# Kernel optimization log

Hardware: AMD Instinct MI355X
Metric: run time of the kernel (lower is better)

## Reference

```python
import jax, jax.numpy as jnp
import numpy as np
from jax import lax

DIM = 64
HEADS = 4
B, H, W = 4, 256, 256


def _conv(x, w, b, pad, groups=1):
    y = lax.conv_general_dilated(x, w, (1, 1), [(pad, pad), (pad, pad)],
                                 dimension_numbers=('NCHW', 'OIHW', 'NCHW'),
                                 feature_group_count=groups)
    return y + b[None, :, None, None]


def _ckbd_mask(h, w, anchor):
    ii = jnp.arange(h)[:, None]
    jj = jnp.arange(w)[None, :]
    par = (ii + jj) % 2
    return (par == 1) if anchor else (par == 0)


def ckbd_anchor(y):
    return y * _ckbd_mask(y.shape[2], y.shape[3], True)


def ckbd_nonanchor(y):
    return y * _ckbd_mask(y.shape[2], y.shape[3], False)


def anchor_squeeze(y):
    b, c, h, w = y.shape
    even = y[:, :, 0::2, 1::2]  # anchor cells on even rows
    odd = y[:, :, 1::2, 0::2]   # anchor cells on odd rows
    return jnp.stack([even, odd], axis=3).reshape(b, c, h, w // 2)


def nonanchor_squeeze(y):
    b, c, h, w = y.shape
    even = y[:, :, 0::2, 0::2]
    odd = y[:, :, 1::2, 1::2]
    return jnp.stack([even, odd], axis=3).reshape(b, c, h, w // 2)


def anchor_unsqueeze(y):
    b, c, h, wh = y.shape
    out = jnp.zeros((b, c, h, wh * 2), y.dtype)
    out = out.at[:, :, 0::2, 1::2].set(y[:, :, 0::2, :])
    out = out.at[:, :, 1::2, 0::2].set(y[:, :, 1::2, :])
    return out


def nonanchor_unsqueeze(y):
    b, c, h, wh = y.shape
    out = jnp.zeros((b, c, h, wh * 2), y.dtype)
    out = out.at[:, :, 0::2, 0::2].set(y[:, :, 0::2, :])
    out = out.at[:, :, 1::2, 1::2].set(y[:, :, 1::2, :])
    return out


def setup_inputs() -> dict:
    key = jax.random.key(0)
    ks = jax.random.split(key, 16)
    s = 0.05
    C = DIM
    nrm = lambda k, shp: jax.random.normal(k, shp, jnp.float32) * s
    z = lambda n: jnp.zeros((n,), jnp.float32)
    return {
        'x1': jax.random.normal(ks[0], (B, C, H, W), jnp.float32),
        'x2': jax.random.normal(ks[1], (B, C, H, W), jnp.float32),
        'q1_w': nrm(ks[2], (C, C, 1, 1)), 'q1_b': z(C),
        'q2_w': nrm(ks[3], (C, 1, 3, 3)), 'q2_b': z(C),
        'k1_w': nrm(ks[4], (C, C, 1, 1)), 'k1_b': z(C),
        'k2_w': nrm(ks[5], (C, 1, 3, 3)), 'k2_b': z(C),
        'v1_w': nrm(ks[6], (C, C, 1, 1)), 'v1_b': z(C),
        'v2_w': nrm(ks[7], (C, 1, 3, 3)), 'v2_b': z(C),
        'r_w': nrm(ks[8], (2 * C, C, 5, 5)), 'r_b': z(2 * C),
        'm1_w': nrm(ks[9], (4 * C, 2 * C, 1, 1)), 'm1_b': z(4 * C),
        'm2_w': nrm(ks[10], (4 * C, 1, 3, 3)), 'm2_b': z(4 * C),
        'm3_w': nrm(ks[11], (2 * C, 4 * C, 1, 1)), 'm3_b': z(2 * C),
    }


def reference(x1, x2, q1_w, q1_b, q2_w, q2_b, k1_w, k1_b, k2_w, k2_b,
              v1_w, v1_b, v2_w, v2_b, r_w, r_b,
              m1_w, m1_b, m2_w, m2_b, m3_w, m3_b):
    C = DIM
    b, _, h, w = x1.shape
    d = C // HEADS
    x1_ac = ckbd_anchor(x1)
    x1_na = ckbd_nonanchor(x1)
    # QKV: 1x1 conv then depthwise 3x3
    q = _conv(_conv(x1_na, q1_w, q1_b, 0), q2_w, q2_b, 1, groups=C)
    k = _conv(_conv(x1_ac, k1_w, k1_b, 0), k2_w, k2_b, 1, groups=C)
    v = _conv(_conv(x2, v1_w, v1_b, 0), v2_w, v2_b, 1, groups=C)
    q = nonanchor_squeeze(q)  # (b, C, h, w//2)
    k = anchor_squeeze(k)
    v = anchor_squeeze(v)
    # per-head softmaxes: key over spatial, query over head channels
    kh = k.reshape(b, HEADS, d, h * (w // 2))
    qh = q.reshape(b, HEADS, d, h, w // 2)
    kh = jax.nn.softmax(kh, axis=-1).reshape(b, HEADS, d, h, w // 2)
    qh = jax.nn.softmax(qh, axis=2)
    vh = v.reshape(b, HEADS, d, h, w // 2)
    # scatter back to full grid (zeros off-pattern), flatten spatial
    kf = anchor_unsqueeze(kh.reshape(b, C, h, w // 2)).reshape(b, HEADS, d, h * w)
    vf = anchor_unsqueeze(vh.reshape(b, C, h, w // 2)).reshape(b, HEADS, d, h * w)
    qf = nonanchor_unsqueeze(qh.reshape(b, C, h, w // 2)).reshape(b, HEADS, d, h * w)
    # linear attention: context = K @ V^T (d x d), out = context^T @ Q
    ctx = jnp.einsum('bhdn,bhen->bhde', kf, vf)
    att = jnp.einsum('bhde,bhdn->bhen', ctx, qf).reshape(b, C, h, w)
    attention = _conv(att, r_w, r_b, 2)
    m = jax.nn.gelu(_conv(attention, m1_w, m1_b, 0), approximate=False)
    m = jax.nn.gelu(_conv(m, m2_w, m2_b, 1, groups=4 * C), approximate=False)
    m = _conv(m, m3_w, m3_b, 0)
    return attention + m
```

## Files before the change

kernel.cpp:

```cpp
#include <hip/hip_runtime.h>
#include <hip/hip_bf16.h>
#include <cstdint>

#define NHW 65536
#define NSQ 32768

static constexpr size_t OFF_AQ  = 0;
static constexpr size_t OFF_AK  = 8388608;
static constexpr size_t OFF_AV  = 16777216;
static constexpr size_t OFF_EK  = 33554432;
static constexpr size_t OFF_VD  = 41943040;
static constexpr size_t OFF_ATT = 50331648;
static constexpr size_t OFF_CTX = 58720256;
static constexpr size_t OFF_Z   = 58724352;
static constexpr size_t OFF_RWT = 58724608;
static constexpr size_t MB2_US  = 67108864;
static constexpr size_t A16_US  = 67108864;
static constexpr size_t W6_US   = 117654016;
static constexpr size_t W8_US   = 0;

typedef __attribute__((ext_vector_type(8))) short short8;
typedef __attribute__((ext_vector_type(4))) float floatx4;

__device__ __constant__ int TKH[25] = {0,0,0,1,1,2,2,2,3,3,4,4,4,  0,0,1,1,1,2,2,3,3,3,4,4};
__device__ __constant__ int TKW[25] = {0,2,4,1,3,0,2,4,1,3,0,2,4,  1,3,0,2,4,1,3,0,2,4,1,3};

__device__ __forceinline__ float geluf(float x) {
  return 0.5f * x * (1.0f + erff(x * 0.70710678118654752440f));
}
__device__ __forceinline__ unsigned short f2bf(float f) {
  union { float f; uint32_t u; } v; v.f = f;
  uint32_t x = v.u;
  uint32_t r = x + 0x7fffu + ((x >> 16) & 1u);
  return (unsigned short)(r >> 16);
}
__device__ __forceinline__ float bf2f(unsigned short u) {
  union { uint32_t i; float f; } v; v.i = ((uint32_t)u) << 16; return v.f;
}

__global__ void __launch_bounds__(256) k0_wprep(const float* __restrict__ rw,
                                                unsigned short* __restrict__ wAu) {
  int idx = blockIdx.x * 256 + threadIdx.x;
  int cj = idx & 7, o = (idx >> 3) & 127, chunk = (idx >> 10) & 7, tap = idx >> 13;
  int c = chunk * 8 + cj;
  int t = TKH[tap] * 5 + TKW[tap];
  wAu[idx] = f2bf(rw[(o * 64 + c) * 25 + t]);
}

__global__ void __launch_bounds__(256) k0b_w6(const float* __restrict__ m1w,
                                              unsigned short* __restrict__ w6) {
  int idx = blockIdx.x * 256 + threadIdx.x;
  int cj = idx & 7, o = (idx >> 3) & 255, chunk = idx >> 11;
  w6[idx] = f2bf(m1w[o * 128 + chunk * 8 + cj]);
}

__global__ void __launch_bounds__(256) k0c_w8(const float* __restrict__ m3w,
                                              unsigned short* __restrict__ w8) {
  int idx = blockIdx.x * 256 + threadIdx.x;
  int cj = idx & 7, o = (idx >> 3) & 127, chunk = idx >> 10;
  w8[idx] = f2bf(m3w[o * 256 + chunk * 8 + cj]);
}

__global__ void __launch_bounds__(256) k1_qkv(
    const float* __restrict__ x1, const float* __restrict__ x2,
    const float* __restrict__ q1w, const float* __restrict__ q1b,
    const float* __restrict__ k1w, const float* __restrict__ k1b,
    const float* __restrict__ v1w, const float* __restrict__ v1b,
    float* ws) {
  __shared__ float wq[4096], wk[4096], wv[4096];
  int tid = threadIdx.x;
  for (int idx = tid; idx < 4096; idx += 256) {
    int o = idx >> 6, c = idx & 63;
    wq[c * 64 + o] = q1w[o * 64 + c];
    wk[c * 64 + o] = k1w[o * 64 + c];
    wv[c * 64 + o] = v1w[o * 64 + c];
  }
  __syncthreads();
  int b = blockIdx.x >> 8, i = blockIdx.x & 255;
  int w = tid >> 6, l = tid & 63;
  int j = (((w >> 1) * 64 + l) << 1) | (w & 1);
  int par = (i + j) & 1;
  const float* wsel = par ? wk : wq;
  const float* bsel = par ? k1b : q1b;
  float acc[64];
#pragma unroll
  for (int o = 0; o < 64; o++) acc[o] = bsel[o];
  const float* xp = x1 + ((size_t)b * 64) * NHW + i * 256 + j;
  for (int c = 0; c < 64; c++) {
    float v = xp[(size_t)c * NHW];
    const float* wr = wsel + c * 64;
#pragma unroll
    for (int o = 0; o < 64; o++) acc[o] += wr[o] * v;
  }
  {
    float* dst = ws + (par ? OFF_AK : OFF_AQ) + ((size_t)b * 64) * NSQ + i * 128 + (j >> 1);
#pragma unroll
    for (int o = 0; o < 64; o++) dst[(size_t)o * NSQ] = acc[o];
  }
#pragma unroll
  for (int o = 0; o < 64; o++) acc[o] = v1b[o];
  const float* xp2 = x2 + ((size_t)b * 64) * NHW + i * 256 + j;
  for (int c = 0; c < 64; c++) {
    float v = xp2[(size_t)c * NHW];
    const float* wr = wv + c * 64;
#pragma unroll
    for (int o = 0; o < 64; o++) acc[o] += wr[o] * v;
  }
  float* dv = ws + OFF_AV + ((size_t)b * 64) * NHW + i * 256 + j;
#pragma unroll
  for (int o = 0; o < 64; o++) dv[(size_t)o * NHW] = acc[o];
}

__global__ void __launch_bounds__(256) k2_dw(
    float* ws,
    const float* __restrict__ kw2, const float* __restrict__ kb2, const float* __restrict__ kb1,
    const float* __restrict__ vw2, const float* __restrict__ vb2) {
  int ig = blockIdx.x, c = blockIdx.y, b = blockIdx.z;
  int i0 = ig * 16;
  int tid = threadIdx.x;

  __shared__ float akL[18][130];
  __shared__ float avL[18][260];
  __shared__ float red[256];

  const float* AKg = ws + OFF_AK + ((size_t)(b * 64 + c)) * NSQ;
  const float* AVg = ws + OFF_AV + ((size_t)(b * 64 + c)) * NHW;

  for (int idx = tid; idx < 18 * 128; idx += 256) {
    int r = idx >> 7, col = idx & 127;
    int gi = i0 - 1 + r;
    akL[r][1 + col] = (gi >= 0 && gi < 256) ? AKg[gi * 128 + col] : 0.f;
  }
  for (int idx = tid; idx < 18 * 256; idx += 256) {
    int r = idx >> 8, col = idx & 255;
    int gi = i0 - 1 + r;
    avL[r][1 + col] = (gi >= 0 && gi < 256) ? AVg[gi * 256 + col] : 0.f;
  }
  if (tid < 18) {
    akL[tid][0] = 0.f; akL[tid][129] = 0.f;
    avL[tid][0] = 0.f; avL[tid][257] = 0.f;
  }
  __syncthreads();

  int tr = tid >> 4, tj = tid & 15;
  int i = i0 + tr;
  int jp0 = tj * 8;
  int li = tr + 1;
  int s = 1 - (i & 1);

  const float* w9 = kw2 + c * 9;
  float kw0 = w9[0], kw1 = w9[1], kw2c = w9[2], kw3 = w9[3], kw4 = w9[4],
        kw5 = w9[5], kw6 = w9[6], kw7 = w9[7], kw8 = w9[8];
  float kb2c = kb2[c], kb1c = kb1[c];
  const float* vwp = vw2 + c * 9;
  float vw0 = vwp[0], vw1 = vwp[1], vw2v = vwp[2], vw3 = vwp[3], vw4 = vwp[4],
        vw5 = vwp[5], vw6 = vwp[6], vw7 = vwp[7], vw8 = vwp[8];
  float vbc = vb2[c];

  float ek[8], vd[8];
  float zsum = 0.f;
#pragma unroll
  for (int u = 0; u < 8; u++) {
    int jp = jp0 + u;
    int j = 2 * jp + s;
    float bs = 0.f;
    if (i > 0)   bs += kw1;
    if (i < 255) bs += kw7;
    if (j > 0)   bs += kw3;
    if (j < 255) bs += kw5;
    float acc = kb2c + kb1c * bs
      + kw4 * akL[li][1 + jp]
      + kw0 * akL[li - 1][jp + s] + kw2c * akL[li - 1][1 + jp + s]
      + kw6 * akL[li + 1][jp + s] + kw8 * akL[li + 1][1 + jp + s];
    float e = expf(acc);
    ek[u] = e; zsum += e;
    vd[u] = vbc
      + vw0 * avL[li - 1][j] + vw1 * avL[li - 1][1 + j] + vw2v * avL[li - 1][2 + j]
      + vw3 * avL[li    ][j] + vw4 * avL[li    ][1 + j] + vw5  * avL[li    ][2 + j]
      + vw6 * avL[li + 1][j] + vw7 * avL[li + 1][1 + j] + vw8  * avL[li + 1][2 + j];
  }

  float* ekp = ws + OFF_EK + ((size_t)(b * 64 + c)) * NSQ + i * 128 + jp0;
  float* vdp = ws + OFF_VD + ((size_t)(b * 64 + c)) * NSQ + i * 128 + jp0;
  float4 e0 = {ek[0], ek[1], ek[2], ek[3]}, e1 = {ek[4], ek[5], ek[6], ek[7]};
  float4 v0 = {vd[0], vd[1], vd[2], vd[3]}, v1 = {vd[4], vd[5], vd[6], vd[7]};
  *(float4*)(ekp) = e0; *(float4*)(ekp + 4) = e1;
  *(float4*)(vdp) = v0; *(float4*)(vdp + 4) = v1;

  red[tid] = zsum;
  __syncthreads();
#pragma unroll
  for (int off = 128; off > 0; off >>= 1) {
    if (tid < off) red[tid] += red[tid + off];
    __syncthreads();
  }
  if (tid == 0) atomicAdd(ws + OFF_Z + (b * 64 + c), red[0]);
}

__global__ void __launch_bounds__(256) k3_ctx(float* ws) {
  int bid = blockIdx.x;
  int b = bid >> 5, h = (bid >> 3) & 3, ch = bid & 7;
  int n0 = ch * 4096;
  int tid = threadIdx.x;
  int d = tid >> 4, e = tid & 15;
  __shared__ float ekt[16][260];
  __shared__ float vdt[16][260];
  const float* ekb = ws + OFF_EK + ((size_t)(b * 64 + h * 16)) * NSQ + n0;
  const float* vdb = ws + OFF_VD + ((size_t)(b * 64 + h * 16)) * NSQ + n0;
  float acc = 0.f;
  for (int sub = 0; sub < 16; sub++) {
    __syncthreads();
#pragma unroll
    for (int r = 0; r < 16; r++) {
      ekt[r][tid] = ekb[(size_t)r * NSQ + sub * 256 + tid];
      vdt[r][tid] = vdb[(size_t)r * NSQ + sub * 256 + tid];
    }
    __syncthreads();
#pragma unroll 8
    for (int x = 0; x < 256; x++) acc += ekt[d][x] * vdt[e][x];
  }
  atomicAdd(ws + OFF_CTX + ((b * 4 + h) * 16 + d) * 16 + e, acc);
}

__global__ void __launch_bounds__(256) k4_att(
    float* ws,
    const float* __restrict__ qw2, const float* __restrict__ qb2, const float* __restrict__ qb1) {
  int b = blockIdx.x >> 7, ip = blockIdx.x & 127;
  int tid = threadIdx.x;
  int i = ip * 2 + (tid >> 7);
  int jp = tid & 127;
  __shared__ float ctxn[1024];
  for (int idx = tid; idx < 1024; idx += 256)
    ctxn[idx] = ws[OFF_CTX + b * 1024 + idx] / ws[OFF_Z + b * 64 + (idx >> 4)];
  __syncthreads();
  int s = i & 1;
  int j = 2 * jp + s;
  int cl = jp - 1 + s, cr = jp + s;
  unsigned short* attB = (unsigned short*)(ws + OFF_ATT);
  unsigned short* dstp = attB + (((size_t)(b * 256 + i)) * 128 + jp) * 64;
  for (int h = 0; h < 4; h++) {
    float qv[16];
#pragma unroll
    for (int dc = 0; dc < 16; dc++) {
      int c = h * 16 + dc;
      const float* AQ = ws + OFF_AQ + ((size_t)(b * 64 + c)) * NSQ;
      const float* w9 = qw2 + c * 9;
      float acc = qb2[c] + w9[4] * AQ[i * 128 + jp];
      if (i > 0) {
        const float* r = AQ + (i - 1) * 128;
        if (cl >= 0)   acc += w9[0] * r[cl];
        if (cr <= 127) acc += w9[2] * r[cr];
      }
      if (i < 255) {
        const float* r = AQ + (i + 1) * 128;
        if (cl >= 0)   acc += w9[6] * r[cl];
        if (cr <= 127) acc += w9[8] * r[cr];
      }
      float bs = 0.f;
      if (i > 0)   bs += w9[1];
      if (i < 255) bs += w9[7];
      if (j > 0)   bs += w9[3];
      if (j < 255) bs += w9[5];
      qv[dc] = acc + qb1[c] * bs;
    }
    float mx = qv[0];
#pragma unroll
    for (int dc = 1; dc < 16; dc++) mx = fmaxf(mx, qv[dc]);
    float sum = 0.f;
#pragma unroll
    for (int dc = 0; dc < 16; dc++) { qv[dc] = expf(qv[dc] - mx); sum += qv[dc]; }
    float inv = 1.0f / sum;
#pragma unroll
    for (int e = 0; e < 16; e++) {
      float a = 0.f;
#pragma unroll
      for (int dc = 0; dc < 16; dc++) a += ctxn[h * 256 + dc * 16 + e] * qv[dc];
      dstp[h * 16 + e] = f2bf(a * inv);
    }
  }
}

__global__ void __launch_bounds__(256) k5_mfma(
    const unsigned short* __restrict__ attB, const unsigned short* __restrict__ wAu,
    const float* __restrict__ rb, float* __restrict__ out,
    unsigned short* __restrict__ a16) {
  int p = blockIdx.y, b = blockIdx.z;
  int i0 = (blockIdx.x >> 2) * 4;
  int jp0 = (blockIdx.x & 3) * 32;
  int tid = threadIdx.x;
  int wv = tid >> 6, lane = tid & 63;
  int mh = wv & 1, nh = wv >> 1;
  int l15 = lane & 15, quad = lane >> 4;

  __shared__ __align__(16) unsigned short attL[24576];
  __shared__ __align__(16) unsigned short wL[8192];

  const unsigned short* attBase = attB + ((size_t)b * 256) * 128 * 64;
  for (int k = 0; k < 12; k++) {
    int u = k * 256 + tid;
    int chunk = u & 7;
    int pos = (u >> 3) & 15;
    int cbr = u >> 7;
    int cb = cbr % 3, lr = cbr / 3;
    int r = i0 - 2 + lr;
    int jp = jp0 - 2 + cb * 16 + pos;
    short8 v = {0, 0, 0, 0, 0, 0, 0, 0};
    if (r >= 0 && r < 256 && jp >= 0 && jp < 128)
      v = *(const short8*)(attBase + (((size_t)r * 128) + jp) * 64 + chunk * 8);
    int slot = chunk ^ (pos & 7);
    *(short8*)(attL + (((size_t)cbr * 16 + pos) * 8 + slot) * 8) = v;
  }

  floatx4 acc[16];
#pragma unroll
  for (int x = 0; x < 16; x++) acc[x] = floatx4{0.f, 0.f, 0.f, 0.f};

  int riv[4], ci2[4];
#pragma unroll
  for (int nt = 0; nt < 4; nt++) {
    int ntg = nh * 4 + nt;
    riv[nt] = ntg >> 1;
    ci2[nt] = (ntg & 1) * 16 + l15 + 2;
  }

  int t0 = p ? 13 : 0;
  int ntaps = p ? 12 : 13;
  for (int tt = 0; tt < ntaps; tt++) {
    int tap = t0 + tt;
    int kh = TKH[tap], kw = TKW[tap];
    __syncthreads();
    {
      const short8* src = (const short8*)(wAu + (size_t)tap * 8192);
      short8* dst = (short8*)wL;
#pragma unroll
      for (int k = 0; k < 4; k++) dst[k * 256 + tid] = src[k * 256 + tid];
    }
    __syncthreads();
#pragma unroll
    for (int chalf = 0; chalf < 2; chalf++) {
      short8 a[4], bf[4];
#pragma unroll
      for (int mt = 0; mt < 4; mt++)
        a[mt] = *(const short8*)(wL + (((chalf * 4 + quad) * 128) + mh * 64 + mt * 16 + l15) * 8);
#pragma unroll
      for (int nt = 0; nt < 4; nt++) {
        int lr = riv[nt] + kh;
        int off = ((kw - 2) + ((p + riv[nt]) & 1) - ((riv[nt] + kh) & 1)) >> 1;
        int lc = ci2[nt] + off;
        int cb = lc >> 4, pos = lc & 15;
        int slot = (chalf * 4 + quad) ^ (pos & 7);
        bf[nt] = *(const short8*)(attL + ((((lr * 3 + cb) * 16 + pos) * 8) + slot) * 8);
      }
#pragma unroll
      for (int mt = 0; mt < 4; mt++)
#pragma unroll
        for (int nt = 0; nt < 4; nt++)
          acc[mt * 4 + nt] =
              __builtin_amdgcn_mfma_f32_16x16x32_bf16(a[mt], bf[nt], acc[mt * 4 + nt], 0, 0, 0);
    }
  }

#pragma unroll
  for (int mt = 0; mt < 4; mt++) {
#pragma unroll
    for (int nt = 0; nt < 4; nt++) {
      int ntg = nh * 4 + nt;
      int i = i0 + (ntg >> 1);
      int jp = jp0 + (ntg & 1) * 16 + l15;
      int j = 2 * jp + ((p + i) & 1);
      floatx4 v = acc[mt * 4 + nt];
      int o0 = mh * 64 + mt * 16 + quad * 4;
      ushort4 u4;
      float r0 = v[0] + rb[o0 + 0];
      float r1 = v[1] + rb[o0 + 1];
      float r2 = v[2] + rb[o0 + 2];
      float r3 = v[3] + rb[o0 + 3];
      out[(((size_t)(b * 128 + o0 + 0)) * 256 + i) * 256 + j] = r0;
      out[(((size_t)(b * 128 + o0 + 1)) * 256 + i) * 256 + j] = r1;
      out[(((size_t)(b * 128 + o0 + 2)) * 256 + i) * 256 + j] = r2;
      out[(((size_t)(b * 128 + o0 + 3)) * 256 + i) * 256 + j] = r3;
      u4.x = f2bf(r0); u4.y = f2bf(r1); u4.z = f2bf(r2); u4.w = f2bf(r3);
      *(ushort4*)(a16 + ((size_t)b * 65536 + (size_t)i * 256 + j) * 128 + o0) = u4;
    }
  }
}

__global__ void __launch_bounds__(256) k6_m1(
    const unsigned short* __restrict__ a16, const unsigned short* __restrict__ w6,
    const float* __restrict__ m1b, unsigned short* __restrict__ mb) {
  int px0 = blockIdx.x * 128;
  int og = blockIdx.y, b = blockIdx.z;
  int tid = threadIdx.x;
  int wv = tid >> 6, lane = tid & 63;
  int mh = wv & 1, nh = wv >> 1;
  int l15 = lane & 15, quad = lane >> 4;
  __shared__ __align__(16) unsigned short attL[16384];

  const unsigned short* src = a16 + ((size_t)b * 65536 + px0) * 128;
#pragma unroll
  for (int k = 0; k < 8; k++) {
    int u = k * 256 + tid;
    int n = u >> 4, chunk = u & 15;
    short8 v = *(const short8*)(src + (size_t)n * 128 + chunk * 8);
    int slot = chunk ^ (n & 7);
    *(short8*)(attL + ((size_t)n * 16 + slot) * 8) = v;
  }
  __syncthreads();

  floatx4 acc[16];
#pragma unroll
  for (int x = 0; x < 16; x++) acc[x] = floatx4{0.f, 0.f, 0.f, 0.f};

#pragma unroll
  for (int step = 0; step < 4; step++) {
    int chunk = step * 4 + quad;
    short8 aw[4], bp[4];
#pragma unroll
    for (int mt = 0; mt < 4; mt++) {
      int o = og * 128 + mh * 64 + mt * 16 + l15;
      aw[mt] = *(const short8*)(w6 + ((size_t)chunk * 256 + o) * 8);
    }
#pragma unroll
    for (int nt = 0; nt < 4; nt++) {
      int row = nh * 64 + nt * 16 + l15;
      int slot = chunk ^ (row & 7);
      bp[nt] = *(const short8*)(attL + (row * 16 + slot) * 8);
    }
#pragma unroll
    for (int mt = 0; mt < 4; mt++)
#pragma unroll
      for (int nt = 0; nt < 4; nt++)
        acc[mt * 4 + nt] =
            __builtin_amdgcn_mfma_f32_16x16x32_bf16(aw[mt], bp[nt], acc[mt * 4 + nt], 0, 0, 0);
  }

#pragma unroll
  for (int mt = 0; mt < 4; mt++) {
    int o0 = og * 128 + mh * 64 + mt * 16 + quad * 4;
    float4 bo = *(const float4*)(m1b + o0);
#pragma unroll
    for (int nt = 0; nt < 4; nt++) {
      int px = px0 + nh * 64 + nt * 16 + l15;
      floatx4 v = acc[mt * 4 + nt];
      ushort4 u;
      u.x = f2bf(geluf(v[0] + bo.x));
      u.y = f2bf(geluf(v[1] + bo.y));
      u.z = f2bf(geluf(v[2] + bo.z));
      u.w = f2bf(geluf(v[3] + bo.w));
      *(ushort4*)(mb + ((size_t)b * 65536 + px) * 256 + o0) = u;
    }
  }
}

__global__ void __launch_bounds__(256) k7_m2(
    const unsigned short* __restrict__ mb, const float* __restrict__ m2w,
    const float* __restrict__ m2b, unsigned short* __restrict__ mb2) {
  int b = blockIdx.y;
  int i0 = (blockIdx.x >> 2) * 4;
  int jq = blockIdx.x & 3;
  int t = threadIdx.x;
  int l = t & 63, ri = t >> 6;
  int co = l * 4;
  int i = i0 + ri;
  int j0 = jq * 64;
  const unsigned short* ibase = mb + ((size_t)b * 65536) * 256 + co;
  unsigned short* obase = mb2 + ((size_t)b * 65536) * 256 + co;

  float w[9][4], bias[4];
#pragma unroll
  for (int cc = 0; cc < 4; cc++) {
    bias[cc] = m2b[co + cc];
#pragma unroll
    for (int tap = 0; tap < 9; tap++) w[tap][cc] = m2w[(co + cc) * 9 + tap];
  }

  float wA[3][4], wB[3][4], wC[3][4];

#define K7_LOAD(dst, ir, jc)                                                        \
  do {                                                                              \
    if ((unsigned)(ir) < 256u && (unsigned)(jc) < 256u) {                           \
      ushort4 u_ = *(const ushort4*)(ibase + ((size_t)((ir) * 256 + (jc))) * 256);  \
      dst[0] = bf2f(u_.x); dst[1] = bf2f(u_.y);                                     \
      dst[2] = bf2f(u_.z); dst[3] = bf2f(u_.w);                                     \
    } else {                                                                        \
      dst[0] = 0.f; dst[1] = 0.f; dst[2] = 0.f; dst[3] = 0.f;                       \
    }                                                                               \
  } while (0)

#pragma unroll
  for (int r = 0; r < 3; r++) {
    K7_LOAD(wA[r], i - 1 + r, j0 - 1);
    K7_LOAD(wB[r], i - 1 + r, j0);
  }

  for (int j = j0; j < j0 + 64; j++) {
#pragma unroll
    for (int r = 0; r < 3; r++) K7_LOAD(wC[r], i - 1 + r, j + 1);
    float acc[4];
#pragma unroll
    for (int cc = 0; cc < 4; cc++) {
      acc[cc] = bias[cc]
        + w[0][cc] * wA[0][cc] + w[1][cc] * wB[0][cc] + w[2][cc] * wC[0][cc]
        + w[3][cc] * wA[1][cc] + w[4][cc] * wB[1][cc] + w[5][cc] * wC[1][cc]
        + w[6][cc] * wA[2][cc] + w[7][cc] * wB[2][cc] + w[8][cc] * wC[2][cc];
    }
    ushort4 u;
    u.x = f2bf(geluf(acc[0]));
    u.y = f2bf(geluf(acc[1]));
    u.z = f2bf(geluf(acc[2]));
    u.w = f2bf(geluf(acc[3]));
    *(ushort4*)(obase + ((size_t)(i * 256 + j)) * 256) = u;
#pragma unroll
    for (int r = 0; r < 3; r++) {
#pragma unroll
      for (int cc = 0; cc < 4; cc++) { wA[r][cc] = wB[r][cc]; wB[r][cc] = wC[r][cc]; }
    }
  }
#undef K7_LOAD
}

__global__ void __launch_bounds__(256) k8_m3(
    const unsigned short* __restrict__ mb2, const unsigned short* __restrict__ w8,
    const float* __restrict__ m3b, float* __restrict__ out) {
  int px0 = blockIdx.x * 128;
  int b = blockIdx.z;
  int tid = threadIdx.x;
  int wv = tid >> 6, lane = tid & 63;
  int mh = wv & 1, nh = wv >> 1;
  int l15 = lane & 15, quad = lane >> 4;
  __shared__ __align__(16) unsigned short attL[16384];

  floatx4 acc[16];
#pragma unroll
  for (int x = 0; x < 16; x++) acc[x] = floatx4{0.f, 0.f, 0.f, 0.f};

  for (int kk = 0; kk < 2; kk++) {
    if (kk) __syncthreads();
    const unsigned short* src = mb2 + ((size_t)b * 65536 + px0) * 256 + kk * 128;
#pragma unroll
    for (int k = 0; k < 8; k++) {
      int u = k * 256 + tid;
      int n = u >> 4, ch = u & 15;
      short8 v = *(const short8*)(src + (size_t)n * 256 + ch * 8);
      int slot = ch ^ (n & 7);
      *(short8*)(attL + ((size_t)n * 16 + slot) * 8) = v;
    }
    __syncthreads();

#pragma unroll
    for (int step = 0; step < 4; step++) {
      int ch = step * 4 + quad;
      int chg = kk * 16 + ch;
      short8 aw[4], bp[4];
#pragma unroll
      for (int mt = 0; mt < 4; mt++) {
        int o = mh * 64 + mt * 16 + l15;
        aw[mt] = *(const short8*)(w8 + ((size_t)chg * 128 + o) * 8);
      }
#pragma unroll
      for (int nt = 0; nt < 4; nt++) {
        int row = nh * 64 + nt * 16 + l15;
        int slot = ch ^ (row & 7);
        bp[nt] = *(const short8*)(attL + (row * 16 + slot) * 8);
      }
#pragma unroll
      for (int mt = 0; mt < 4; mt++)
#pragma unroll
        for (int nt = 0; nt < 4; nt++)
          acc[mt * 4 + nt] =
              __builtin_amdgcn_mfma_f32_16x16x32_bf16(aw[mt], bp[nt], acc[mt * 4 + nt], 0, 0, 0);
    }
  }

#pragma unroll
  for (int mt = 0; mt < 4; mt++) {
    int o0 = mh * 64 + mt * 16 + quad * 4;
    float4 bo = *(const float4*)(m3b + o0);
#pragma unroll
    for (int nt = 0; nt < 4; nt++) {
      int px = px0 + nh * 64 + nt * 16 + l15;
      floatx4 v = acc[mt * 4 + nt];
      size_t a0 = ((size_t)(b * 128 + o0 + 0)) * NHW + px;
      size_t a1 = ((size_t)(b * 128 + o0 + 1)) * NHW + px;
      size_t a2 = ((size_t)(b * 128 + o0 + 2)) * NHW + px;
      size_t a3 = ((size_t)(b * 128 + o0 + 3)) * NHW + px;
      out[a0] += v[0] + bo.x;
      out[a1] += v[1] + bo.y;
      out[a2] += v[2] + bo.z;
      out[a3] += v[3] + bo.w;
    }
  }
}

extern "C" void kernel_launch(void* const* d_in, const int* in_sizes, int n_in,
                              void* d_out, int out_size, void* d_ws, size_t ws_size,
                              hipStream_t stream) {
  const float* x1  = (const float*)d_in[0];
  const float* x2  = (const float*)d_in[1];
  const float* q1w = (const float*)d_in[2];  const float* q1b = (const float*)d_in[3];
  const float* q2w = (const float*)d_in[4];  const float* q2b = (const float*)d_in[5];
  const float* k1w = (const float*)d_in[6];  const float* k1b = (const float*)d_in[7];
  const float* k2w = (const float*)d_in[8];  const float* k2b = (const float*)d_in[9];
  const float* v1w = (const float*)d_in[10]; const float* v1b = (const float*)d_in[11];
  const float* v2w = (const float*)d_in[12]; const float* v2b = (const float*)d_in[13];
  const float* rw  = (const float*)d_in[14]; const float* rb  = (const float*)d_in[15];
  const float* m1w = (const float*)d_in[16]; const float* m1b = (const float*)d_in[17];
  const float* m2w = (const float*)d_in[18]; const float* m2b = (const float*)d_in[19];
  const float* m3w = (const float*)d_in[20]; const float* m3b = (const float*)d_in[21];
  float* ws = (float*)d_ws;
  float* out = (float*)d_out;
  unsigned short* mb  = (unsigned short*)d_ws;
  unsigned short* mb2 = (unsigned short*)d_ws + MB2_US;
  unsigned short* a16 = (unsigned short*)d_ws + A16_US;
  unsigned short* w6  = (unsigned short*)d_ws + W6_US;
  unsigned short* w8  = (unsigned short*)d_ws + W8_US;
  unsigned short* attB = (unsigned short*)(ws + OFF_ATT);
  unsigned short* wAu  = (unsigned short*)(ws + OFF_RWT);

  (void)hipMemsetAsync((char*)d_ws + OFF_CTX * sizeof(float), 0, (4096 + 256) * sizeof(float), stream);
  k0_wprep<<<800, 256, 0, stream>>>(rw, wAu);
  k0b_w6<<<128, 256, 0, stream>>>(m1w, w6);
  k1_qkv<<<1024, 256, 0, stream>>>(x1, x2, q1w, q1b, k1w, k1b, v1w, v1b, ws);
  k2_dw<<<dim3(16, 64, 4), 256, 0, stream>>>(ws, k2w, k2b, k1b, v2w, v2b);
  k3_ctx<<<128, 256, 0, stream>>>(ws);
  k4_att<<<512, 256, 0, stream>>>(ws, q2w, q2b, q1b);
  k5_mfma<<<dim3(256, 2, 4), 256, 0, stream>>>(attB, wAu, rb, out, a16);
  k6_m1<<<dim3(512, 2, 4), 256, 0, stream>>>(a16, w6, m1b, mb);
  k7_m2<<<dim3(256, 4), 256, 0, stream>>>(mb, m2w, m2b, mb2);
  k0c_w8<<<128, 256, 0, stream>>>(m3w, w8);
  k8_m3<<<dim3(512, 1, 4), 256, 0, stream>>>(mb2, w8, m3b, out);
}
```

Baseline: 1.004 ms.

## Rewrite QKV 1x1 projections as bf16 MFMA GEMMs with swizzled LDS tiles

Replaces the scalar fp32 per-thread 64-channel dot products in the QKV projection kernel with bf16 MFMA 16x16x32 matrix ops. Input rows are converted to bf16 and staged in a XOR-swizzled LDS tile, and weights are pre-converted to bf16 by a new prep kernel. Q and K are computed only on their checkerboard-selected columns. This targets the FMA-bound, register-heavy original loop, but lowers projection precision to bf16 and adds a small prep launch.

New measurement: 931.3 us. 7.3% less time.

```diff
diff --git a/kernel.cpp b/kernel.cpp
--- a/kernel.cpp
+++ b/kernel.cpp
@@ -17,6 +17,7 @@
 static constexpr size_t MB2_US  = 67108864;
 static constexpr size_t A16_US  = 67108864;
 static constexpr size_t W6_US   = 117654016;
+static constexpr size_t WQKV_US = 117686784;
 static constexpr size_t W8_US   = 0;
 
 typedef __attribute__((ext_vector_type(8))) short short8;
@@ -61,54 +62,157 @@
   w8[idx] = f2bf(m3w[o * 256 + chunk * 8 + cj]);
 }
 
+__global__ void __launch_bounds__(256) k0d_wqkv(
+    const float* __restrict__ q1w, const float* __restrict__ k1w,
+    const float* __restrict__ v1w, unsigned short* __restrict__ wqkv) {
+  int idx = blockIdx.x * 256 + threadIdx.x;
+  int cj = idx & 7, o = (idx >> 3) & 63, chunk = (idx >> 9) & 7, mat = idx >> 12;
+  const float* src = mat == 0 ? q1w : (mat == 1 ? k1w : v1w);
+  wqkv[idx] = f2bf(src[o * 64 + chunk * 8 + cj]);
+}
+
 __global__ void __launch_bounds__(256) k1_qkv(
     const float* __restrict__ x1, const float* __restrict__ x2,
-    const float* __restrict__ q1w, const float* __restrict__ q1b,
-    const float* __restrict__ k1w, const float* __restrict__ k1b,
-    const float* __restrict__ v1w, const float* __restrict__ v1b,
-    float* ws) {
-  __shared__ float wq[4096], wk[4096], wv[4096];
+    const unsigned short* __restrict__ wqkv,
+    const float* __restrict__ q1b, const float* __restrict__ k1b,
+    const float* __restrict__ v1b, float* ws) {
+  int b = blockIdx.x >> 8, i = blockIdx.x & 255;
   int tid = threadIdx.x;
-  for (int idx = tid; idx < 4096; idx += 256) {
-    int o = idx >> 6, c = idx & 63;
-    wq[c * 64 + o] = q1w[o * 64 + c];
-    wk[c * 64 + o] = k1w[o * 64 + c];
-    wv[c * 64 + o] = v1w[o * 64 + c];
+  int wv = tid >> 6, lane = tid & 63;
+  int mh = wv & 1, nh = wv >> 1;
+  int l15 = lane & 15, quad = lane >> 4;
+  __shared__ __align__(16) unsigned short xL[16384];
+
+  {
+    const float* xr = x1 + ((size_t)b * 64) * NHW + i * 256;
+#pragma unroll
+    for (int u = 0; u < 8; u++) {
+      int idx = u * 256 + tid;
+      int j = idx & 255, chunk = idx >> 8;
+      short8 v;
+#pragma unroll
+      for (int cj = 0; cj < 8; cj++)
+        v[cj] = (short)f2bf(xr[(size_t)(chunk * 8 + cj) * NHW + j]);
+      int slot = chunk ^ ((j >> 1) & 7);
+      *(short8*)(xL + (size_t)(j * 8 + slot) * 8) = v;
+    }
   }
   __syncthreads();
-  int b = blockIdx.x >> 8, i = blockIdx.x & 255;
-  int w = tid >> 6, l = tid & 63;
-  int j = (((w >> 1) * 64 + l) << 1) | (w & 1);
-  int par = (i + j) & 1;
-  const float* wsel = par ? wk : wq;
-  const float* bsel = par ? k1b : q1b;
-  float acc[64];
-#pragma unroll
-  for (int o = 0; o < 64; o++) acc[o] = bsel[o];
-  const float* xp = x1 + ((size_t)b * 64) * NHW + i * 256 + j;
-  for (int c = 0; c < 64; c++) {
-    float v = xp[(size_t)c * NHW];
-    const float* wr = wsel + c * 64;
-#pragma unroll
-    for (int o = 0; o < 64; o++) acc[o] += wr[o] * v;
-  }
+
+  int s_na = i & 1, s_a = 1 - s_na;
+
+  floatx4 accq[8], acck[8];
+#pragma unroll
+  for (int x = 0; x < 8; x++) {
+    accq[x] = floatx4{0.f, 0.f, 0.f, 0.f};
+    acck[x] = floatx4{0.f, 0.f, 0.f, 0.f};
+  }
+
+#pragma unroll
+  for (int chalf = 0; chalf < 2; chalf++) {
+    int chunk = chalf * 4 + quad;
+    short8 awq[2], awk[2], bq[4], bk[4];
+#pragma unroll
+    for (int mt = 0; mt < 2; mt++) {
+      int o = mh * 32 + mt * 16 + l15;
+      awq[mt] = *(const short8*)(wqkv + ((size_t)(0 * 8 + chunk) * 64 + o) * 8);
+      awk[mt] = *(const short8*)(wqkv + ((size_t)(1 * 8 + chunk) * 64 + o) * 8);
+    }
+#pragma unroll
+    for (int nt = 0; nt < 4; nt++) {
+      int jp = nh * 64 + nt * 16 + l15;
+      int slot = chunk ^ (jp & 7);
+      int jq = 2 * jp + s_na, jk = 2 * jp + s_a;
+      bq[nt] = *(const short8*)(xL + (size_t)(jq * 8 + slot) * 8);
+      bk[nt] = *(const short8*)(xL + (size_t)(jk * 8 + slot) * 8);
+    }
+#pragma unroll
+    for (int mt = 0; mt < 2; mt++)
+#pragma unroll
+      for (int nt = 0; nt < 4; nt++) {
+        accq[mt * 4 + nt] =
+            __builtin_amdgcn_mfma_f32_16x16x32_bf16(awq[mt], bq[nt], accq[mt * 4 + nt], 0, 0, 0);
+        acck[mt * 4 + nt] =
+            __builtin_amdgcn_mfma_f32_16x16x32_bf16(awk[mt], bk[nt], acck[mt * 4 + nt], 0, 0, 0);
+      }
+  }
+
+#pragma unroll
+  for (int mt = 0; mt < 2; mt++) {
+    int o0 = mh * 32 + mt * 16 + quad * 4;
+    float4 bq4 = *(const float4*)(q1b + o0);
+    float4 bk4 = *(const float4*)(k1b + o0);
+#pragma unroll
+    for (int nt = 0; nt < 4; nt++) {
+      int jp = nh * 64 + nt * 16 + l15;
+      floatx4 vq = accq[mt * 4 + nt];
+      floatx4 vk = acck[mt * 4 + nt];
+      float* dq = ws + OFF_AQ + ((size_t)(b * 64 + o0)) * NSQ + i * 128 + jp;
+      float* dk = ws + OFF_AK + ((size_t)(b * 64 + o0)) * NSQ + i * 128 + jp;
+      dq[0 * NSQ] = vq[0] + bq4.x; dq[1 * NSQ] = vq[1] + bq4.y;
+      dq[2 * NSQ] = vq[2] + bq4.z; dq[3 * NSQ] = vq[3] + bq4.w;
+      dk[0 * NSQ] = vk[0] + bk4.x; dk[1 * NSQ] = vk[1] + bk4.y;
+      dk[2 * NSQ] = vk[2] + bk4.z; dk[3 * NSQ] = vk[3] + bk4.w;
+    }
+  }
+
+  __syncthreads();
   {
-    float* dst = ws + (par ? OFF_AK : OFF_AQ) + ((size_t)b * 64) * NSQ + i * 128 + (j >> 1);
-#pragma unroll
-    for (int o = 0; o < 64; o++) dst[(size_t)o * NSQ] = acc[o];
-  }
-#pragma unroll
-  for (int o = 0; o < 64; o++) acc[o] = v1b[o];
-  const float* xp2 = x2 + ((size_t)b * 64) * NHW + i * 256 + j;
-  for (int c = 0; c < 64; c++) {
-    float v = xp2[(size_t)c * NHW];
-    const float* wr = wv + c * 64;
-#pragma unroll
-    for (int o = 0; o < 64; o++) acc[o] += wr[o] * v;
-  }
-  float* dv = ws + OFF_AV + ((size_t)b * 64) * NHW + i * 256 + j;
-#pragma unroll
-  for (int o = 0; o < 64; o++) dv[(size_t)o * NHW] = acc[o];
+    const float* xr = x2 + ((size_t)b * 64) * NHW + i * 256;
+#pragma unroll
+    for (int u = 0; u < 8; u++) {
+      int idx = u * 256 + tid;
+      int j = idx & 255, chunk = idx >> 8;
+      short8 v;
+#pragma unroll
+      for (int cj = 0; cj < 8; cj++)
+        v[cj] = (short)f2bf(xr[(size_t)(chunk * 8 + cj) * NHW + j]);
+      int slot = chunk ^ ((j >> 1) & 7);
+      *(short8*)(xL + (size_t)(j * 8 + slot) * 8) = v;
+    }
+  }
+  __syncthreads();
+
+  floatx4 accv[16];
+#pragma unroll
+  for (int x = 0; x < 16; x++) accv[x] = floatx4{0.f, 0.f, 0.f, 0.f};
+
+#pragma unroll
+  for (int chalf = 0; chalf < 2; chalf++) {
+    int chunk = chalf * 4 + quad;
+    short8 awv[2], bv[8];
+#pragma unroll
+    for (int mt = 0; mt < 2; mt++) {
+      int o = mh * 32 + mt * 16 + l15;
+      awv[mt] = *(const short8*)(wqkv + ((size_t)(2 * 8 + chunk) * 64 + o) * 8);
+    }
+#pragma unroll
+    for (int nt = 0; nt < 8; nt++) {
+      int j = nh * 128 + nt * 16 + l15;
+      int slot = chunk ^ ((j >> 1) & 7);
+      bv[nt] = *(const short8*)(xL + (size_t)(j * 8 + slot) * 8);
+    }
+#pragma unroll
+    for (int mt = 0; mt < 2; mt++)
+#pragma unroll
+      for (int nt = 0; nt < 8; nt++)
+        accv[mt * 8 + nt] =
+            __builtin_amdgcn_mfma_f32_16x16x32_bf16(awv[mt], bv[nt], accv[mt * 8 + nt], 0, 0, 0);
+  }
+
+#pragma unroll
+  for (int mt = 0; mt < 2; mt++) {
+    int o0 = mh * 32 + mt * 16 + quad * 4;
+    float4 bv4 = *(const float4*)(v1b + o0);
+#pragma unroll
+    for (int nt = 0; nt < 8; nt++) {
+      int j = nh * 128 + nt * 16 + l15;
+      floatx4 vv = accv[mt * 8 + nt];
+      float* dv = ws + OFF_AV + ((size_t)(b * 64 + o0)) * NHW + i * 256 + j;
+      dv[0 * NHW] = vv[0] + bv4.x; dv[1 * NHW] = vv[1] + bv4.y;
+      dv[2 * NHW] = vv[2] + bv4.z; dv[3 * NHW] = vv[3] + bv4.w;
+    }
+  }
 }
 
 __global__ void __launch_bounds__(256) k2_dw(
@@ -613,6 +717,7 @@
   unsigned short* mb2 = (unsigned short*)d_ws + MB2_US;
   unsigned short* a16 = (unsigned short*)d_ws + A16_US;
   unsigned short* w6  = (unsigned short*)d_ws + W6_US;
+  unsigned short* wqkv = (unsigned short*)d_ws + WQKV_US;
   unsigned short* w8  = (unsigned short*)d_ws + W8_US;
   unsigned short* attB = (unsigned short*)(ws + OFF_ATT);
   unsigned short* wAu  = (unsigned short*)(ws + OFF_RWT);
@@ -620,7 +725,8 @@
   (void)hipMemsetAsync((char*)d_ws + OFF_CTX * sizeof(float), 0, (4096 + 256) * sizeof(float), stream);
   k0_wprep<<<800, 256, 0, stream>>>(rw, wAu);
   k0b_w6<<<128, 256, 0, stream>>>(m1w, w6);
-  k1_qkv<<<1024, 256, 0, stream>>>(x1, x2, q1w, q1b, k1w, k1b, v1w, v1b, ws);
+  k0d_wqkv<<<48, 256, 0, stream>>>(q1w, k1w, v1w, wqkv);
+  k1_qkv<<<1024, 256, 0, stream>>>(x1, x2, wqkv, q1b, k1b, v1b, ws);
   k2_dw<<<dim3(16, 64, 4), 256, 0, stream>>>(ws, k2w, k2b, k1b, v2w, v2b);
   k3_ctx<<<128, 256, 0, stream>>>(ws);
   k4_att<<<512, 256, 0, stream>>>(ws, q2w, q2b, q1b);
```
